# Kernel tuning notes

Hardware: AMD Instinct MI355X
Metric: run time of the kernel (lower is better)

Reference implementation:

```python
import jax, jax.numpy as jnp
import numpy as np

H, D, KD, E = 8, 128, 16, 128
B, G = 16, 501

def setup_inputs() -> dict:
    key = jax.random.key(0)
    ks = jax.random.split(key, 12)
    stdv = 1.0 / np.sqrt(KD)
    u = lambda k, shape, s: jax.random.uniform(k, shape, jnp.float32, -s, s)
    inp = {"q": jax.random.normal(ks[0], (B, G, D), jnp.float32)}
    names = ["W_query", "W_key", "W_val", "W1_query", "W2_query", "W3_query",
             "W4_query", "W5_query", "W6_query"]
    for i, n in enumerate(names):
        inp[n] = u(ks[i + 1], (H, D, KD), stdv)
    inp["W_out"] = u(ks[10], (H, KD, E), 1.0 / np.sqrt(E))
    return inp

def _forward(q, W_query, W_key, W_val, W1, W2, W3, W4, W5, W6, W_out):
    h = q  # self-attention: h defaults to q
    b, g, d = h.shape
    np_ = (g - 1) // 2
    norm = 1.0 / jnp.sqrt(jnp.float32(KD))
    pick = h[:, 1:np_ + 1]          # [b, np, d]
    delivery = h[:, np_ + 1:]       # [b, np, d]
    proj = lambda x, W: jnp.einsum('bnd,hdk->hbnk', x, W)
    Q = proj(q, W_query); K = proj(h, W_key); V = proj(h, W_val)
    K_pick = proj(pick, W_key); V_pick = proj(pick, W_val)
    K_del = proj(delivery, W_key); V_del = proj(delivery, W_val)
    Q_pick = proj(pick, W1); Q_pick_ap = proj(pick, W2); Q_pick_ad = proj(pick, W3)
    Q_del = proj(delivery, W4); Q_del_ad = proj(delivery, W5); Q_del_ap = proj(delivery, W6)

    comp = norm * jnp.einsum('hbqk,hbgk->hbqg', Q, K)                 # [h,b,g,g]
    c_pd = norm * jnp.sum(Q_pick * K_del, -1)                          # [h,b,np]
    c_p_ap = norm * jnp.einsum('hbqk,hbpk->hbqp', Q_pick_ap, K_pick)   # [h,b,np,np]
    c_p_ad = norm * jnp.einsum('hbqk,hbpk->hbqp', Q_pick_ad, K_del)
    c_dp = norm * jnp.sum(Q_del * K_pick, -1)                          # [h,b,np]
    c_d_ad = norm * jnp.einsum('hbqk,hbpk->hbqp', Q_del_ad, K_del)
    c_d_ap = norm * jnp.einsum('hbqk,hbpk->hbqp', Q_del_ap, K_pick)

    ninf = lambda *s: jnp.full(s, -jnp.inf, comp.dtype)
    # pad branch scores to query length g (depot row + wrong-subset rows = -inf)
    c_add_del = jnp.concatenate([ninf(H, b, 1), c_pd, ninf(H, b, np_)], -1)[..., None]            # [h,b,g,1]
    c_add_ap = jnp.concatenate([ninf(H, b, 1, np_), c_p_ap, ninf(H, b, np_, np_)], 2)             # [h,b,g,np]
    c_add_ad = jnp.concatenate([ninf(H, b, 1, np_), c_p_ad, ninf(H, b, np_, np_)], 2)
    c_add_pick = jnp.concatenate([ninf(H, b, 1), ninf(H, b, np_), c_dp], -1)[..., None]
    c_add_ad2 = jnp.concatenate([ninf(H, b, 1, np_), ninf(H, b, np_, np_), c_d_ad], 2)
    c_add_ap2 = jnp.concatenate([ninf(H, b, 1, np_), ninf(H, b, np_, np_), c_d_ap], 2)
    comp_full = jnp.concatenate([comp, c_add_del, c_add_ap, c_add_ad,
                                 c_add_pick, c_add_ad2, c_add_ap2], -1)  # [h,b,g,g+2+4*np]

    attn = jax.nn.softmax(comp_full, axis=-1)

    z = lambda *s: jnp.zeros(s, V.dtype)
    V_add_del = jnp.concatenate([z(H, b, 1, KD), V_del, z(H, b, np_, KD)], 2)   # [h,b,g,kd]
    V_add_pick = jnp.concatenate([z(H, b, 1, KD), z(H, b, np_, KD), V_pick], 2)

    mm = lambda a, v: jnp.einsum('hbqp,hbpk->hbqk', a, v)
    heads = mm(attn[..., :g], V)
    heads = heads + attn[..., g:g + 1] * V_add_del
    heads = heads + mm(attn[..., g + 1:g + 1 + np_], V_pick)
    heads = heads + mm(attn[..., g + 1 + np_:g + 1 + 2 * np_], V_del)
    heads = heads + attn[..., g + 1 + 2 * np_:g + 2 + 2 * np_] * V_add_pick
    heads = heads + mm(attn[..., g + 2 + 2 * np_:g + 2 + 3 * np_], V_del)
    heads = heads + mm(attn[..., g + 2 + 3 * np_:], V_pick)

    return jnp.einsum('hbnk,hke->bne', heads, W_out)

def reference(q, W_query, W_key, W_val, W1_query, W2_query, W3_query,
              W4_query, W5_query, W6_query, W_out):
    return _forward(q, W_query, W_key, W_val, W1_query, W2_query, W3_query,
                    W4_query, W5_query, W6_query, W_out)
```

## Files before the change

kernel.cpp:

```cpp
#include <hip/hip_runtime.h>

#define H_ 8
#define D_ 128
#define KD_ 16
#define E_ 128
#define B_ 16
#define G_ 501
#define NP_ 250
#define BN_ (B_*G_)

typedef __bf16 bf16x8 __attribute__((ext_vector_type(8)));
typedef float f32x4 __attribute__((ext_vector_type(4)));
typedef unsigned short u16x8 __attribute__((ext_vector_type(8)));
typedef unsigned short u16x4 __attribute__((ext_vector_type(4)));
typedef bf16x8 __attribute__((may_alias)) bf16x8_a;
typedef u16x8 __attribute__((may_alias)) u16x8_a;
typedef u16x4 __attribute__((may_alias)) u16x4_a;

__device__ __forceinline__ unsigned short f2bf(float f) {
  unsigned int u = __builtin_bit_cast(unsigned int, f);
  unsigned int r = u + 0x7FFFu + ((u >> 16) & 1u);
  return (unsigned short)(r >> 16);
}
__device__ __forceinline__ float bf2f(unsigned short u) {
  unsigned int v = ((unsigned int)u) << 16;
  return __builtin_bit_cast(float, v);
}

__global__ __launch_bounds__(256) void k_prep(
    const float* __restrict__ w0, const float* __restrict__ w1, const float* __restrict__ w2,
    const float* __restrict__ w3, const float* __restrict__ w4, const float* __restrict__ w5,
    const float* __restrict__ w6, const float* __restrict__ w7, const float* __restrict__ w8,
    unsigned short* __restrict__ wct, unsigned short* __restrict__ Pvt) {
  int i = blockIdx.x * 256 + threadIdx.x;
  if (i < H_*9*KD_*D_) {
    int d = i & 127; int t = i >> 7; int k = t & 15; t >>= 4;
    int wi = t % 9; int h = t / 9;
    const float* src = w0;
    switch (wi) {
      case 1: src = w1; break; case 2: src = w2; break; case 3: src = w3; break;
      case 4: src = w4; break; case 5: src = w5; break; case 6: src = w6; break;
      case 7: src = w7; break; case 8: src = w8; break; default: break;
    }
    wct[i] = f2bf(src[h*(D_*KD_) + d*KD_ + k]);
  }
  if (i < 128*16*19) {
    int s = i / 304; int r2 = i - s*304; int k = r2 / 19; int key = 501 + (r2 - k*19);
    Pvt[(size_t)s*8320 + k*520 + key] = 0;
  }
}

__global__ __launch_bounds__(256) void k_proj(const float* __restrict__ q,
                                              const unsigned short* __restrict__ wct,
                                              unsigned short* __restrict__ P,
                                              unsigned short* __restrict__ Pvt) {
  const int tid = threadIdx.x;
  const int lane = tid & 63;
  const int wv = tid >> 6;
  const int ln = lane & 15;
  const int quad = lane >> 4;
  const int b = blockIdx.y >> 3;
  const int nt = blockIdx.y & 7;
  const int cbase = blockIdx.x * 64;

  __shared__ __align__(16) unsigned short sA[64*136];
  __shared__ __align__(16) unsigned short sB[64*136];

  for (int i = tid; i < 1024; i += 256) {
    int rr = i >> 4, half = i & 15;
    int r = min(nt*64 + rr, G_ - 1);
    const float* src = q + (size_t)(b*G_ + r)*D_ + half*8;
    float4 f0 = ((const float4*)src)[0];
    float4 f1 = ((const float4*)src)[1];
    u16x8 v;
    v[0]=f2bf(f0.x); v[1]=f2bf(f0.y); v[2]=f2bf(f0.z); v[3]=f2bf(f0.w);
    v[4]=f2bf(f1.x); v[5]=f2bf(f1.y); v[6]=f2bf(f1.z); v[7]=f2bf(f1.w);
    *(u16x8*)(sA + rr*136 + half*8) = v;
  }
  for (int i = tid; i < 1024; i += 256) {
    int cc = i >> 4, half = i & 15;
    u16x8 v = *(const u16x8*)(wct + (size_t)(cbase + cc)*D_ + half*8);
    *(u16x8*)(sB + cc*136 + half*8) = v;
  }
  __syncthreads();

  bf16x8 a[4];
  #pragma unroll
  for (int ks = 0; ks < 4; ++ks)
    a[ks] = *(const bf16x8_a*)(sA + (wv*16 + ln)*136 + ks*32 + quad*8);

  #pragma unroll
  for (int ct = 0; ct < 4; ++ct) {
    f32x4 acc = {0.f,0.f,0.f,0.f};
    #pragma unroll
    for (int ks = 0; ks < 4; ++ks) {
      bf16x8 bb = *(const bf16x8_a*)(sB + (ct*16 + ln)*136 + ks*32 + quad*8);
      acc = __builtin_amdgcn_mfma_f32_16x16x32_bf16(a[ks], bb, acc, 0,0,0);
    }
    const int c = cbase + ct*16 + ln;
    const int h = c / 144; const int rem = c - h*144; const int w = rem >> 4; const int k = rem & 15;
    if (w == 2) {
      unsigned short* dstv = Pvt + (size_t)(h*B_ + b)*8320 + k*520;
      #pragma unroll
      for (int g = 0; g < 4; ++g) {
        const int nn = nt*64 + wv*16 + quad*4 + g;
        if (nn < G_) dstv[nn] = f2bf(acc[g]);
      }
    } else {
      const float sc = (w == 1) ? 1.0f : 0.25f;
      const size_t pb = ((size_t)((h*9 + w)*B_ + b)*G_)*KD_ + k;
      #pragma unroll
      for (int g = 0; g < 4; ++g) {
        const int nn = nt*64 + wv*16 + quad*4 + g;
        if (nn < G_) P[pb + (size_t)nn*KD_] = f2bf(acc[g]*sc);
      }
    }
  }
}

__device__ __forceinline__ f32x4 mf(bf16x8 a, bf16x8 b, f32x4 c) {
  return __builtin_amdgcn_mfma_f32_16x16x32_bf16(a, b, c, 0,0,0);
}

__device__ __forceinline__ void score_chunk(
    int c, bool up, bool dn, int cbuf,
    const unsigned short* sK, bf16x8 qa, bf16x8 qp, bf16x8 qdl,
    unsigned short* eb, float rv, float& esum, int ln, int quad)
{
  const f32x4 z4 = {0.f,0.f,0.f,0.f};
  bf16x8 k0 = {}, k1 = {};
  if (quad < 2) {
    const unsigned short* kp = sK + (c*32 + ln)*24 + quad*8;
    k0 = *(const bf16x8_a*)(kp);
    k1 = *(const bf16x8_a*)(kp + 384);
  }
  f32x4 sa0 = mf(k0, qa, z4), sa1 = mf(k1, qa, z4);
  f32x4 sp0 = z4, sp1 = z4, sd0 = z4, sd1 = z4;
  if (up) { sp0 = mf(k0, qp, z4);  sp1 = mf(k1, qp, z4); }
  if (dn) { sd0 = mf(k0, qdl, z4); sd1 = mf(k1, qdl, z4); }

  float el = 0.f;
  unsigned short ev[8];
  #pragma unroll
  for (int t = 0; t < 2; ++t) {
    #pragma unroll
    for (int rg = 0; rg < 4; ++rg) {
      float comp = __expf(t ? sa1[rg] : sa0[rg]);
      if (c == 15 && t == 1) comp *= (quad*4 + rg <= 4) ? 1.f : 0.f;
      float ex = 0.f;
      if (up) {
        float m = 1.f;
        if (c == 0 && t == 0 && rg == 0) m = (quad != 0) ? 1.f : 0.f;
        if (c == 7 && t == 1) m = (quad*4 + rg <= 10) ? 1.f : 0.f;
        ex += m * __expf(t ? sp1[rg] : sp0[rg]);
      }
      if (dn) {
        float m = 1.f;
        if (c == 7)  m = (t == 1 && quad*4 + rg >= 11) ? 1.f : 0.f;
        if (c == 15 && t == 1) m = (quad*4 + rg <= 4) ? 1.f : 0.f;
        ex += m * __expf(t ? sd1[rg] : sd0[rg]);
      }
      float e = comp + rv * ex;
      el += e;
      ev[t*4 + rg] = f2bf(e);
    }
  }
  esum += el;
  u16x4 w0, w1;
  w0[0]=ev[0]; w0[1]=ev[1]; w0[2]=ev[2]; w0[3]=ev[3];
  w1[0]=ev[4]; w1[1]=ev[5]; w1[2]=ev[6]; w1[3]=ev[7];
  unsigned short* base = eb + cbuf*640 + ln*40 + quad*4;
  *(u16x4_a*)(base)      = w0;
  *(u16x4_a*)(base + 16) = w1;
}

__global__ __launch_bounds__(256, 2) void k_attn(const unsigned short* __restrict__ P,
                                                 const unsigned short* __restrict__ Pvt,
                                                 unsigned short* __restrict__ headsb) {
  const int rt2 = blockIdx.x, b = blockIdx.y, h = blockIdx.z;
  const int tid = threadIdx.x;
  const int lane = tid & 63;
  const int wv = tid >> 6;
  const int ln = lane & 15;
  const int quad = lane >> 4;

  __shared__ __align__(16) unsigned short sK [512*24];
  __shared__ __align__(16) unsigned short sVt[16*520];
  __shared__ __align__(16) unsigned short sQ [8*1040];
  __shared__ __align__(16) unsigned short eBuf[4*2*640];

  const size_t slab = (size_t)G_*KD_;
  const unsigned short* Pk = P + ((size_t)(h*9+1)*B_ + b)*slab;
  const u16x8 vz = {0,0,0,0,0,0,0,0};

  for (int i = tid; i < 1024; i += 256) {
    int key = i >> 1, half = i & 1;
    u16x8 v = vz;
    if (key < G_) v = *(const u16x8*)(Pk + key*KD_ + half*8);
    *(u16x8*)(sK + key*24 + half*8) = v;
  }
  const unsigned short* pv = Pvt + (size_t)(h*B_ + b)*8320;
  for (int i = tid; i < 1040; i += 256)
    *(u16x8*)(sVt + i*8) = *(const u16x8*)(pv + i*8);
  for (int i = tid; i < 1040; i += 256) {
    int t = i / 520; int j2 = i - t*520;
    int arr = j2 / 130; int j = j2 - arr*130;
    int rr = j >> 1, half = j & 1;
    int r = (rt2*2 + t)*64 + rr;
    u16x8 v = vz;
    if (rr < 64 && r < G_) {
      bool pick = (r <= NP_);
      int w = (arr==0) ? 0 : (arr==1) ? (pick?4:8) : (arr==2) ? (pick?5:7) : (pick?3:6);
      v = *(const u16x8*)(P + ((size_t)(h*9+w)*B_ + b)*slab + (size_t)r*KD_ + half*8);
    }
    *(u16x8*)(sQ + (t*4+arr)*1040 + j*8) = v;
  }
  __syncthreads();

  unsigned short* eb = eBuf + wv*1280;

  for (int t = 0; t < 2; ++t) {
    const int r0 = (rt2*2 + t)*64;
    const unsigned short* sQt = sQ + t*4160;
    const int aoff = (wv*16 + ln)*16 + quad*8;
    bf16x8 qa  = *(const bf16x8_a*)(sQt + aoff);
    bf16x8 qp  = *(const bf16x8_a*)(sQt + 1040 + aoff);
    bf16x8 qdl = *(const bf16x8_a*)(sQt + 2080 + aoff);

    const int ra = r0 + wv*16 + ln;
    const float rv = (ra >= 1) ? 1.f : 0.f;

    f32x4 acc = {0.f,0.f,0.f,0.f};
    float esum = 0.f;

    #pragma unroll
    for (int p = 0; p < 8; ++p) {
      const int c0 = 2*p, c1 = c0 + 1;
      score_chunk(c0, c0 <= 7, c0 >= 7, 0, sK, qa, qp, qdl, eb, rv, esum, ln, quad);
      score_chunk(c1, c1 <= 7, c1 >= 7, 1, sK, qa, qp, qdl, eb, rv, esum, ln, quad);
      #pragma unroll
      for (int u = 0; u < 2; ++u) {
        bf16x8 Ef = *(const bf16x8_a*)(eb + u*640 + ln*40 + quad*8);
        bf16x8 Vf = *(const bf16x8_a*)(sVt + ln*520 + (c0+u)*32 + quad*8);
        acc = mf(Vf, Ef, acc);
      }
    }

    esum += __shfl_xor(esum, 16);
    esum += __shfl_xor(esum, 32);

    const unsigned short* qsp = sQt + 3120 + (wv*16 + ln)*16;
    const int kpair = (ra >= 1 && ra < G_) ? ((ra <= NP_) ? ra + NP_ : ra - NP_) : 0;
    const unsigned short* ksp = sK + kpair*24;
    u16x8 qs0 = *(const u16x8_a*)(qsp), qs1 = *(const u16x8_a*)(qsp + 8);
    u16x8 ks0 = *(const u16x8_a*)(ksp), ks1 = *(const u16x8_a*)(ksp + 8);
    float s = 0.f;
    #pragma unroll
    for (int kd = 0; kd < 8; ++kd) {
      s = fmaf(bf2f(qs0[kd]), bf2f(ks0[kd]), s);
      s = fmaf(bf2f(qs1[kd]), bf2f(ks1[kd]), s);
    }
    const float rvs = (ra >= 1 && ra < G_) ? 1.f : 0.f;
    const float esng = rvs * __expf(s);
    const float rcp = __builtin_amdgcn_rcpf(esum + esng);

    u16x4 ov;
    ov[0] = f2bf((acc[0] + esng * bf2f(sVt[(quad*4+0)*520 + kpair])) * rcp);
    ov[1] = f2bf((acc[1] + esng * bf2f(sVt[(quad*4+1)*520 + kpair])) * rcp);
    ov[2] = f2bf((acc[2] + esng * bf2f(sVt[(quad*4+2)*520 + kpair])) * rcp);
    ov[3] = f2bf((acc[3] + esng * bf2f(sVt[(quad*4+3)*520 + kpair])) * rcp);
    if (ra < G_)
      *(u16x4*)(headsb + ((size_t)(b*G_ + ra))*E_ + h*16 + quad*4) = ov;
  }
}

__global__ __launch_bounds__(256) void k_out(const unsigned short* __restrict__ headsb,
                                             const float* __restrict__ wout,
                                             float* __restrict__ out) {
  const int tid = threadIdx.x;
  const int lane = tid & 63;
  const int wv = tid >> 6;
  const int ln = lane & 15;
  const int quad = lane >> 4;
  const int base = blockIdx.x * 64;

  __shared__ __align__(16) unsigned short sWt[128*136];
  for (int i = tid; i < 16384; i += 256) {
    int k = i >> 7, e = i & 127;
    sWt[e*136 + k] = f2bf(wout[i]);
  }
  __syncthreads();

  const int row = min(base + wv*16 + ln, BN_ - 1);
  bf16x8 a[4];
  #pragma unroll
  for (int ks = 0; ks < 4; ++ks)
    a[ks] = *(const bf16x8_a*)(headsb + (size_t)row*E_ + ks*32 + quad*8);

  #pragma unroll
  for (int ct = 0; ct < 8; ++ct) {
    f32x4 acc = {0.f,0.f,0.f,0.f};
    #pragma unroll
    for (int ks = 0; ks < 4; ++ks) {
      bf16x8 bb = *(const bf16x8_a*)(sWt + (ct*16 + ln)*136 + ks*32 + quad*8);
      acc = __builtin_amdgcn_mfma_f32_16x16x32_bf16(a[ks], bb, acc, 0,0,0);
    }
    #pragma unroll
    for (int g = 0; g < 4; ++g) {
      const int r = base + wv*16 + quad*4 + g;
      if (r < BN_) out[(size_t)r*E_ + ct*16 + ln] = acc[g];
    }
  }
}

extern "C" void kernel_launch(void* const* d_in, const int* in_sizes, int n_in,
                              void* d_out, int out_size, void* d_ws, size_t ws_size,
                              hipStream_t stream) {
  const float* q = (const float*)d_in[0];
  const float* w0 = (const float*)d_in[1];
  const float* w1 = (const float*)d_in[2];
  const float* w2 = (const float*)d_in[3];
  const float* w3 = (const float*)d_in[4];
  const float* w4 = (const float*)d_in[5];
  const float* w5 = (const float*)d_in[6];
  const float* w6 = (const float*)d_in[7];
  const float* w7 = (const float*)d_in[8];
  const float* w8 = (const float*)d_in[9];
  const float* wout = (const float*)d_in[10];
  float* out = (float*)d_out;

  char* ws = (char*)d_ws;
  unsigned short* wct    = (unsigned short*)(ws);
  unsigned short* P      = (unsigned short*)(ws + 294912);
  unsigned short* Pvt    = (unsigned short*)(ws + 18763776);
  unsigned short* headsb = (unsigned short*)(ws + 20893696);

  k_prep<<<dim3(576), dim3(256), 0, stream>>>(w0,w1,w2,w3,w4,w5,w6,w7,w8, wct, Pvt);
  k_proj<<<dim3(18, 128), dim3(256), 0, stream>>>(q, wct, P, Pvt);
  k_attn<<<dim3(4, 16, 8), dim3(256), 0, stream>>>(P, Pvt, headsb);
  k_out<<<dim3(126), dim3(256), 0, stream>>>(headsb, wout, out);
}
```

Measured before the change: 123.4 us.

## Fuse all stages into one cooperative persistent kernel with grid syncs

Replaces the four separate launches (prep, projection, attention, output) with a single cooperative kernel of 256 blocks that walks the stages in order and separates them with grid-wide syncs. The q-to-bf16 conversion moves into the prep phase and is written to a new workspace buffer. The attention stage now stages score chunks through a single per-wave buffer instead of a double buffer. The aim is to remove launch overheads and inter-kernel gaps. The cost is that the grid is capped at 256 blocks, so the attention and projection tiles are looped over fewer blocks, and the grid syncs add latency.

```diff
diff --git a/kernel.cpp b/kernel.cpp
--- a/kernel.cpp
+++ b/kernel.cpp
@@ -1,4 +1,7 @@
 #include <hip/hip_runtime.h>
+#include <hip/hip_cooperative_groups.h>
+
+namespace cg = cooperative_groups;
 
 #define H_ 8
 #define D_ 128
@@ -27,103 +30,12 @@
   return __builtin_bit_cast(float, v);
 }
 
-__global__ __launch_bounds__(256) void k_prep(
-    const float* __restrict__ w0, const float* __restrict__ w1, const float* __restrict__ w2,
-    const float* __restrict__ w3, const float* __restrict__ w4, const float* __restrict__ w5,
-    const float* __restrict__ w6, const float* __restrict__ w7, const float* __restrict__ w8,
-    unsigned short* __restrict__ wct, unsigned short* __restrict__ Pvt) {
-  int i = blockIdx.x * 256 + threadIdx.x;
-  if (i < H_*9*KD_*D_) {
-    int d = i & 127; int t = i >> 7; int k = t & 15; t >>= 4;
-    int wi = t % 9; int h = t / 9;
-    const float* src = w0;
-    switch (wi) {
-      case 1: src = w1; break; case 2: src = w2; break; case 3: src = w3; break;
-      case 4: src = w4; break; case 5: src = w5; break; case 6: src = w6; break;
-      case 7: src = w7; break; case 8: src = w8; break; default: break;
-    }
-    wct[i] = f2bf(src[h*(D_*KD_) + d*KD_ + k]);
-  }
-  if (i < 128*16*19) {
-    int s = i / 304; int r2 = i - s*304; int k = r2 / 19; int key = 501 + (r2 - k*19);
-    Pvt[(size_t)s*8320 + k*520 + key] = 0;
-  }
-}
-
-__global__ __launch_bounds__(256) void k_proj(const float* __restrict__ q,
-                                              const unsigned short* __restrict__ wct,
-                                              unsigned short* __restrict__ P,
-                                              unsigned short* __restrict__ Pvt) {
-  const int tid = threadIdx.x;
-  const int lane = tid & 63;
-  const int wv = tid >> 6;
-  const int ln = lane & 15;
-  const int quad = lane >> 4;
-  const int b = blockIdx.y >> 3;
-  const int nt = blockIdx.y & 7;
-  const int cbase = blockIdx.x * 64;
-
-  __shared__ __align__(16) unsigned short sA[64*136];
-  __shared__ __align__(16) unsigned short sB[64*136];
-
-  for (int i = tid; i < 1024; i += 256) {
-    int rr = i >> 4, half = i & 15;
-    int r = min(nt*64 + rr, G_ - 1);
-    const float* src = q + (size_t)(b*G_ + r)*D_ + half*8;
-    float4 f0 = ((const float4*)src)[0];
-    float4 f1 = ((const float4*)src)[1];
-    u16x8 v;
-    v[0]=f2bf(f0.x); v[1]=f2bf(f0.y); v[2]=f2bf(f0.z); v[3]=f2bf(f0.w);
-    v[4]=f2bf(f1.x); v[5]=f2bf(f1.y); v[6]=f2bf(f1.z); v[7]=f2bf(f1.w);
-    *(u16x8*)(sA + rr*136 + half*8) = v;
-  }
-  for (int i = tid; i < 1024; i += 256) {
-    int cc = i >> 4, half = i & 15;
-    u16x8 v = *(const u16x8*)(wct + (size_t)(cbase + cc)*D_ + half*8);
-    *(u16x8*)(sB + cc*136 + half*8) = v;
-  }
-  __syncthreads();
-
-  bf16x8 a[4];
-  #pragma unroll
-  for (int ks = 0; ks < 4; ++ks)
-    a[ks] = *(const bf16x8_a*)(sA + (wv*16 + ln)*136 + ks*32 + quad*8);
-
-  #pragma unroll
-  for (int ct = 0; ct < 4; ++ct) {
-    f32x4 acc = {0.f,0.f,0.f,0.f};
-    #pragma unroll
-    for (int ks = 0; ks < 4; ++ks) {
-      bf16x8 bb = *(const bf16x8_a*)(sB + (ct*16 + ln)*136 + ks*32 + quad*8);
-      acc = __builtin_amdgcn_mfma_f32_16x16x32_bf16(a[ks], bb, acc, 0,0,0);
-    }
-    const int c = cbase + ct*16 + ln;
-    const int h = c / 144; const int rem = c - h*144; const int w = rem >> 4; const int k = rem & 15;
-    if (w == 2) {
-      unsigned short* dstv = Pvt + (size_t)(h*B_ + b)*8320 + k*520;
-      #pragma unroll
-      for (int g = 0; g < 4; ++g) {
-        const int nn = nt*64 + wv*16 + quad*4 + g;
-        if (nn < G_) dstv[nn] = f2bf(acc[g]);
-      }
-    } else {
-      const float sc = (w == 1) ? 1.0f : 0.25f;
-      const size_t pb = ((size_t)((h*9 + w)*B_ + b)*G_)*KD_ + k;
-      #pragma unroll
-      for (int g = 0; g < 4; ++g) {
-        const int nn = nt*64 + wv*16 + quad*4 + g;
-        if (nn < G_) P[pb + (size_t)nn*KD_] = f2bf(acc[g]*sc);
-      }
-    }
-  }
-}
-
 __device__ __forceinline__ f32x4 mf(bf16x8 a, bf16x8 b, f32x4 c) {
   return __builtin_amdgcn_mfma_f32_16x16x32_bf16(a, b, c, 0,0,0);
 }
 
 __device__ __forceinline__ void score_chunk(
-    int c, bool up, bool dn, int cbuf,
+    int c, bool up, bool dn,
     const unsigned short* sK, bf16x8 qa, bf16x8 qp, bf16x8 qdl,
     unsigned short* eb, float rv, float& esum, int ln, int quad)
 {
@@ -169,146 +81,253 @@
   u16x4 w0, w1;
   w0[0]=ev[0]; w0[1]=ev[1]; w0[2]=ev[2]; w0[3]=ev[3];
   w1[0]=ev[4]; w1[1]=ev[5]; w1[2]=ev[6]; w1[3]=ev[7];
-  unsigned short* base = eb + cbuf*640 + ln*40 + quad*4;
+  unsigned short* base = eb + ln*40 + quad*4;
   *(u16x4_a*)(base)      = w0;
   *(u16x4_a*)(base + 16) = w1;
 }
 
-__global__ __launch_bounds__(256, 2) void k_attn(const unsigned short* __restrict__ P,
-                                                 const unsigned short* __restrict__ Pvt,
-                                                 unsigned short* __restrict__ headsb) {
-  const int rt2 = blockIdx.x, b = blockIdx.y, h = blockIdx.z;
+__global__ __launch_bounds__(256, 2) void mega(
+    const float* __restrict__ q,
+    const float* __restrict__ w0, const float* __restrict__ w1, const float* __restrict__ w2,
+    const float* __restrict__ w3, const float* __restrict__ w4, const float* __restrict__ w5,
+    const float* __restrict__ w6, const float* __restrict__ w7, const float* __restrict__ w8,
+    const float* __restrict__ wout,
+    unsigned short* __restrict__ wct, unsigned short* __restrict__ qb,
+    unsigned short* __restrict__ P,   unsigned short* __restrict__ Pvt,
+    unsigned short* __restrict__ headsb, float* __restrict__ out)
+{
+  cg::grid_group gg = cg::this_grid();
+  const int blk = blockIdx.x;
   const int tid = threadIdx.x;
   const int lane = tid & 63;
   const int wv = tid >> 6;
   const int ln = lane & 15;
   const int quad = lane >> 4;
-
-  __shared__ __align__(16) unsigned short sK [512*24];
-  __shared__ __align__(16) unsigned short sVt[16*520];
-  __shared__ __align__(16) unsigned short sQ [8*1040];
-  __shared__ __align__(16) unsigned short eBuf[4*2*640];
-
-  const size_t slab = (size_t)G_*KD_;
-  const unsigned short* Pk = P + ((size_t)(h*9+1)*B_ + b)*slab;
-  const u16x8 vz = {0,0,0,0,0,0,0,0};
-
-  for (int i = tid; i < 1024; i += 256) {
-    int key = i >> 1, half = i & 1;
-    u16x8 v = vz;
-    if (key < G_) v = *(const u16x8*)(Pk + key*KD_ + half*8);
-    *(u16x8*)(sK + key*24 + half*8) = v;
-  }
-  const unsigned short* pv = Pvt + (size_t)(h*B_ + b)*8320;
-  for (int i = tid; i < 1040; i += 256)
-    *(u16x8*)(sVt + i*8) = *(const u16x8*)(pv + i*8);
-  for (int i = tid; i < 1040; i += 256) {
-    int t = i / 520; int j2 = i - t*520;
-    int arr = j2 / 130; int j = j2 - arr*130;
-    int rr = j >> 1, half = j & 1;
-    int r = (rt2*2 + t)*64 + rr;
-    u16x8 v = vz;
-    if (rr < 64 && r < G_) {
-      bool pick = (r <= NP_);
-      int w = (arr==0) ? 0 : (arr==1) ? (pick?4:8) : (arr==2) ? (pick?5:7) : (pick?3:6);
-      v = *(const u16x8*)(P + ((size_t)(h*9+w)*B_ + b)*slab + (size_t)r*KD_ + half*8);
-    }
-    *(u16x8*)(sQ + (t*4+arr)*1040 + j*8) = v;
-  }
-  __syncthreads();
-
-  unsigned short* eb = eBuf + wv*1280;
-
-  for (int t = 0; t < 2; ++t) {
-    const int r0 = (rt2*2 + t)*64;
-    const unsigned short* sQt = sQ + t*4160;
-    const int aoff = (wv*16 + ln)*16 + quad*8;
-    bf16x8 qa  = *(const bf16x8_a*)(sQt + aoff);
-    bf16x8 qp  = *(const bf16x8_a*)(sQt + 1040 + aoff);
-    bf16x8 qdl = *(const bf16x8_a*)(sQt + 2080 + aoff);
-
-    const int ra = r0 + wv*16 + ln;
-    const float rv = (ra >= 1) ? 1.f : 0.f;
-
-    f32x4 acc = {0.f,0.f,0.f,0.f};
-    float esum = 0.f;
-
+  const int gtid = blk*256 + tid;
+  const int T = 256*256;
+
+  __shared__ __align__(16) char smraw[62976];
+  unsigned short* const sm16 = (unsigned short*)smraw;
+
+  for (int i = gtid; i < H_*9*KD_*D_; i += T) {
+    int d = i & 127; int t = i >> 7; int k = t & 15; t >>= 4;
+    int wi = t % 9; int h = t / 9;
+    const float* src = w0;
+    switch (wi) {
+      case 1: src = w1; break; case 2: src = w2; break; case 3: src = w3; break;
+      case 4: src = w4; break; case 5: src = w5; break; case 6: src = w6; break;
+      case 7: src = w7; break; case 8: src = w8; break; default: break;
+    }
+    wct[i] = f2bf(src[h*(D_*KD_) + d*KD_ + k]);
+  }
+  for (int j = gtid; j < BN_*D_/8; j += T) {
+    const float* src = q + (size_t)j*8;
+    float4 f0 = ((const float4*)src)[0];
+    float4 f1 = ((const float4*)src)[1];
+    u16x8 v;
+    v[0]=f2bf(f0.x); v[1]=f2bf(f0.y); v[2]=f2bf(f0.z); v[3]=f2bf(f0.w);
+    v[4]=f2bf(f1.x); v[5]=f2bf(f1.y); v[6]=f2bf(f1.z); v[7]=f2bf(f1.w);
+    *(u16x8*)(qb + (size_t)j*8) = v;
+  }
+  for (int i = gtid; i < 128*16*19; i += T) {
+    int s = i / 304; int r2 = i - s*304; int k = r2 / 19; int key = 501 + (r2 - k*19);
+    Pvt[(size_t)s*8320 + k*520 + key] = 0;
+  }
+  gg.sync();
+
+  {
+    unsigned short* const sA = sm16;
+    unsigned short* const sB = sm16 + 64*136;
+    for (int ti = blk; ti < 2304; ti += 256) {
+      const int x = ti / 128;
+      const int y = ti - x*128;
+      const int b = y >> 3, nt = y & 7;
+      const int cbase = x*64;
+      __syncthreads();
+      for (int i = tid; i < 1024; i += 256) {
+        int rr = i >> 4, half = i & 15;
+        int r = min(nt*64 + rr, G_ - 1);
+        u16x8 v = *(const u16x8*)(qb + (size_t)(b*G_ + r)*D_ + half*8);
+        *(u16x8*)(sA + rr*136 + half*8) = v;
+      }
+      for (int i = tid; i < 1024; i += 256) {
+        int cc = i >> 4, half = i & 15;
+        u16x8 v = *(const u16x8*)(wct + (size_t)(cbase + cc)*D_ + half*8);
+        *(u16x8*)(sB + cc*136 + half*8) = v;
+      }
+      __syncthreads();
+
+      bf16x8 a[4];
+      #pragma unroll
+      for (int ks = 0; ks < 4; ++ks)
+        a[ks] = *(const bf16x8_a*)(sA + (wv*16 + ln)*136 + ks*32 + quad*8);
+
+      #pragma unroll
+      for (int ct = 0; ct < 4; ++ct) {
+        f32x4 acc = {0.f,0.f,0.f,0.f};
+        #pragma unroll
+        for (int ks = 0; ks < 4; ++ks) {
+          bf16x8 bb = *(const bf16x8_a*)(sB + (ct*16 + ln)*136 + ks*32 + quad*8);
+          acc = mf(a[ks], bb, acc);
+        }
+        const int c = cbase + ct*16 + ln;
+        const int h = c / 144; const int rem = c - h*144;
+        const int w = rem >> 4; const int k = rem & 15;
+        if (w == 2) {
+          unsigned short* dstv = Pvt + (size_t)(h*B_ + b)*8320 + k*520;
+          #pragma unroll
+          for (int g = 0; g < 4; ++g) {
+            const int nn = nt*64 + wv*16 + quad*4 + g;
+            if (nn < G_) dstv[nn] = f2bf(acc[g]);
+          }
+        } else {
+          const float sc = (w == 1) ? 1.0f : 0.25f;
+          const size_t pb = ((size_t)((h*9 + w)*B_ + b)*G_)*KD_ + k;
+          #pragma unroll
+          for (int g = 0; g < 4; ++g) {
+            const int nn = nt*64 + wv*16 + quad*4 + g;
+            if (nn < G_) P[pb + (size_t)nn*KD_] = f2bf(acc[g]*sc);
+          }
+        }
+      }
+    }
+  }
+  gg.sync();
+
+  {
+    unsigned short* const sK   = sm16;
+    unsigned short* const sVt  = sm16 + 12288;
+    unsigned short* const sQ   = sm16 + 20608;
+    unsigned short* const eBuf = sm16 + 28928;
+    const size_t slab = (size_t)G_*KD_;
+    const u16x8 vz = {0,0,0,0,0,0,0,0};
+
+    for (int u = blk; u < 512; u += 256) {
+      const int h = u >> 6;
+      const int b = (u >> 2) & 15;
+      const int rt2 = u & 3;
+      const unsigned short* Pk = P + ((size_t)(h*9+1)*B_ + b)*slab;
+
+      __syncthreads();
+      for (int i = tid; i < 1024; i += 256) {
+        int key = i >> 1, half = i & 1;
+        u16x8 v = vz;
+        if (key < G_) v = *(const u16x8*)(Pk + key*KD_ + half*8);
+        *(u16x8*)(sK + key*24 + half*8) = v;
+      }
+      const unsigned short* pv = Pvt + (size_t)(h*B_ + b)*8320;
+      for (int i = tid; i < 1040; i += 256)
+        *(u16x8*)(sVt + i*8) = *(const u16x8*)(pv + i*8);
+      for (int i = tid; i < 1040; i += 256) {
+        int t = i / 520; int j2 = i - t*520;
+        int arr = j2 / 130; int j = j2 - arr*130;
+        int rr = j >> 1, half = j & 1;
+        int r = (rt2*2 + t)*64 + rr;
+        u16x8 v = vz;
+        if (rr < 64 && r < G_) {
+          bool pick = (r <= NP_);
+          int w = (arr==0) ? 0 : (arr==1) ? (pick?4:8) : (arr==2) ? (pick?5:7) : (pick?3:6);
+          v = *(const u16x8*)(P + ((size_t)(h*9+w)*B_ + b)*slab + (size_t)r*KD_ + half*8);
+        }
+        *(u16x8*)(sQ + (t*4+arr)*1040 + j*8) = v;
+      }
+      __syncthreads();
+
+      unsigned short* eb = eBuf + wv*640;
+
+      for (int t = 0; t < 2; ++t) {
+        const int r0 = (rt2*2 + t)*64;
+        const unsigned short* sQt = sQ + t*4160;
+        const int aoff = (wv*16 + ln)*16 + quad*8;
+        bf16x8 qa  = *(const bf16x8_a*)(sQt + aoff);
+        bf16x8 qp  = *(const bf16x8_a*)(sQt + 1040 + aoff);
+        bf16x8 qdl = *(const bf16x8_a*)(sQt + 2080 + aoff);
+
+        const int ra = r0 + wv*16 + ln;
+        const float rv = (ra >= 1) ? 1.f : 0.f;
+
+        f32x4 acc = {0.f,0.f,0.f,0.f};
+        float esum = 0.f;
+
+        #pragma unroll
+        for (int c = 0; c < 7; ++c) {
+          score_chunk(c, true, false, sK, qa, qp, qdl, eb, rv, esum, ln, quad);
+          bf16x8 Ef = *(const bf16x8_a*)(eb + ln*40 + quad*8);
+          bf16x8 Vf = *(const bf16x8_a*)(sVt + ln*520 + c*32 + quad*8);
+          acc = mf(Vf, Ef, acc);
+        }
+        {
+          score_chunk(7, true, true, sK, qa, qp, qdl, eb, rv, esum, ln, quad);
+          bf16x8 Ef = *(const bf16x8_a*)(eb + ln*40 + quad*8);
+          bf16x8 Vf = *(const bf16x8_a*)(sVt + ln*520 + 7*32 + quad*8);
+          acc = mf(Vf, Ef, acc);
+        }
+        #pragma unroll
+        for (int c = 8; c < 16; ++c) {
+          score_chunk(c, false, true, sK, qa, qp, qdl, eb, rv, esum, ln, quad);
+          bf16x8 Ef = *(const bf16x8_a*)(eb + ln*40 + quad*8);
+          bf16x8 Vf = *(const bf16x8_a*)(sVt + ln*520 + c*32 + quad*8);
+          acc = mf(Vf, Ef, acc);
+        }
+
+        esum += __shfl_xor(esum, 16);
+        esum += __shfl_xor(esum, 32);
+
+        const unsigned short* qsp = sQt + 3120 + (wv*16 + ln)*16;
+        const int kpair = (ra >= 1 && ra < G_) ? ((ra <= NP_) ? ra + NP_ : ra - NP_) : 0;
+        const unsigned short* ksp = sK + kpair*24;
+        u16x8 qs0 = *(const u16x8_a*)(qsp), qs1 = *(const u16x8_a*)(qsp + 8);
+        u16x8 ks0 = *(const u16x8_a*)(ksp), ks1 = *(const u16x8_a*)(ksp + 8);
+        float s = 0.f;
+        #pragma unroll
+        for (int kd = 0; kd < 8; ++kd) {
+          s = fmaf(bf2f(qs0[kd]), bf2f(ks0[kd]), s);
+          s = fmaf(bf2f(qs1[kd]), bf2f(ks1[kd]), s);
+        }
+        const float rvs = (ra >= 1 && ra < G_) ? 1.f : 0.f;
+        const float esng = rvs * __expf(s);
+        const float rcp = __builtin_amdgcn_rcpf(esum + esng);
+
+        u16x4 ov;
+        ov[0] = f2bf((acc[0] + esng * bf2f(sVt[(quad*4+0)*520 + kpair])) * rcp);
+        ov[1] = f2bf((acc[1] + esng * bf2f(sVt[(quad*4+1)*520 + kpair])) * rcp);
+        ov[2] = f2bf((acc[2] + esng * bf2f(sVt[(quad*4+2)*520 + kpair])) * rcp);
+        ov[3] = f2bf((acc[3] + esng * bf2f(sVt[(quad*4+3)*520 + kpair])) * rcp);
+        if (ra < G_)
+          *(u16x4*)(headsb + ((size_t)(b*G_ + ra))*E_ + h*16 + quad*4) = ov;
+      }
+    }
+  }
+  gg.sync();
+
+  if (blk < 126) {
+    unsigned short* const sWt = sm16;
+    const int base = blk * 64;
+    for (int i = tid; i < 16384; i += 256) {
+      int k = i >> 7, e = i & 127;
+      sWt[e*136 + k] = f2bf(wout[i]);
+    }
+    __syncthreads();
+
+    const int row = min(base + wv*16 + ln, BN_ - 1);
+    bf16x8 a[4];
     #pragma unroll
-    for (int p = 0; p < 8; ++p) {
-      const int c0 = 2*p, c1 = c0 + 1;
-      score_chunk(c0, c0 <= 7, c0 >= 7, 0, sK, qa, qp, qdl, eb, rv, esum, ln, quad);
-      score_chunk(c1, c1 <= 7, c1 >= 7, 1, sK, qa, qp, qdl, eb, rv, esum, ln, quad);
+    for (int ks = 0; ks < 4; ++ks)
+      a[ks] = *(const bf16x8_a*)(headsb + (size_t)row*E_ + ks*32 + quad*8);
+
+    #pragma unroll
+    for (int ct = 0; ct < 8; ++ct) {
+      f32x4 acc = {0.f,0.f,0.f,0.f};
       #pragma unroll
-      for (int u = 0; u < 2; ++u) {
-        bf16x8 Ef = *(const bf16x8_a*)(eb + u*640 + ln*40 + quad*8);
-        bf16x8 Vf = *(const bf16x8_a*)(sVt + ln*520 + (c0+u)*32 + quad*8);
-        acc = mf(Vf, Ef, acc);
-      }
-    }
-
-    esum += __shfl_xor(esum, 16);
-    esum += __shfl_xor(esum, 32);
-
-    const unsigned short* qsp = sQt + 3120 + (wv*16 + ln)*16;
-    const int kpair = (ra >= 1 && ra < G_) ? ((ra <= NP_) ? ra + NP_ : ra - NP_) : 0;
-    const unsigned short* ksp = sK + kpair*24;
-    u16x8 qs0 = *(const u16x8_a*)(qsp), qs1 = *(const u16x8_a*)(qsp + 8);
-    u16x8 ks0 = *(const u16x8_a*)(ksp), ks1 = *(const u16x8_a*)(ksp + 8);
-    float s = 0.f;
-    #pragma unroll
-    for (int kd = 0; kd < 8; ++kd) {
-      s = fmaf(bf2f(qs0[kd]), bf2f(ks0[kd]), s);
-      s = fmaf(bf2f(qs1[kd]), bf2f(ks1[kd]), s);
-    }
-    const float rvs = (ra >= 1 && ra < G_) ? 1.f : 0.f;
-    const float esng = rvs * __expf(s);
-    const float rcp = __builtin_amdgcn_rcpf(esum + esng);
-
-    u16x4 ov;
-    ov[0] = f2bf((acc[0] + esng * bf2f(sVt[(quad*4+0)*520 + kpair])) * rcp);
-    ov[1] = f2bf((acc[1] + esng * bf2f(sVt[(quad*4+1)*520 + kpair])) * rcp);
-    ov[2] = f2bf((acc[2] + esng * bf2f(sVt[(quad*4+2)*520 + kpair])) * rcp);
-    ov[3] = f2bf((acc[3] + esng * bf2f(sVt[(quad*4+3)*520 + kpair])) * rcp);
-    if (ra < G_)
-      *(u16x4*)(headsb + ((size_t)(b*G_ + ra))*E_ + h*16 + quad*4) = ov;
-  }
-}
-
-__global__ __launch_bounds__(256) void k_out(const unsigned short* __restrict__ headsb,
-                                             const float* __restrict__ wout,
-                                             float* __restrict__ out) {
-  const int tid = threadIdx.x;
-  const int lane = tid & 63;
-  const int wv = tid >> 6;
-  const int ln = lane & 15;
-  const int quad = lane >> 4;
-  const int base = blockIdx.x * 64;
-
-  __shared__ __align__(16) unsigned short sWt[128*136];
-  for (int i = tid; i < 16384; i += 256) {
-    int k = i >> 7, e = i & 127;
-    sWt[e*136 + k] = f2bf(wout[i]);
-  }
-  __syncthreads();
-
-  const int row = min(base + wv*16 + ln, BN_ - 1);
-  bf16x8 a[4];
-  #pragma unroll
-  for (int ks = 0; ks < 4; ++ks)
-    a[ks] = *(const bf16x8_a*)(headsb + (size_t)row*E_ + ks*32 + quad*8);
-
-  #pragma unroll
-  for (int ct = 0; ct < 8; ++ct) {
-    f32x4 acc = {0.f,0.f,0.f,0.f};
-    #pragma unroll
-    for (int ks = 0; ks < 4; ++ks) {
-      bf16x8 bb = *(const bf16x8_a*)(sWt + (ct*16 + ln)*136 + ks*32 + quad*8);
-      acc = __builtin_amdgcn_mfma_f32_16x16x32_bf16(a[ks], bb, acc, 0,0,0);
-    }
-    #pragma unroll
-    for (int g = 0; g < 4; ++g) {
-      const int r = base + wv*16 + quad*4 + g;
-      if (r < BN_) out[(size_t)r*E_ + ct*16 + ln] = acc[g];
+      for (int ks = 0; ks < 4; ++ks) {
+        bf16x8 bb = *(const bf16x8_a*)(sWt + (ct*16 + ln)*136 + ks*32 + quad*8);
+        acc = mf(a[ks], bb, acc);
+      }
+      #pragma unroll
+      for (int g = 0; g < 4; ++g) {
+        const int r = base + wv*16 + quad*4 + g;
+        if (r < BN_) out[(size_t)r*E_ + ct*16 + ln] = acc[g];
+      }
     }
   }
 }
@@ -331,12 +350,15 @@
 
   char* ws = (char*)d_ws;
   unsigned short* wct    = (unsigned short*)(ws);
-  unsigned short* P      = (unsigned short*)(ws + 294912);
-  unsigned short* Pvt    = (unsigned short*)(ws + 18763776);
-  unsigned short* headsb = (unsigned short*)(ws + 20893696);
-
-  k_prep<<<dim3(576), dim3(256), 0, stream>>>(w0,w1,w2,w3,w4,w5,w6,w7,w8, wct, Pvt);
-  k_proj<<<dim3(18, 128), dim3(256), 0, stream>>>(q, wct, P, Pvt);
-  k_attn<<<dim3(4, 16, 8), dim3(256), 0, stream>>>(P, Pvt, headsb);
-  k_out<<<dim3(126), dim3(256), 0, stream>>>(headsb, wout, out);
-}
+  unsigned short* qb     = (unsigned short*)(ws + 294912);
+  unsigned short* P      = (unsigned short*)(ws + 2347008);
+  unsigned short* Pvt    = (unsigned short*)(ws + 20815872);
+  unsigned short* headsb = (unsigned short*)(ws + 22945792);
+
+  void* args[] = {
+    (void*)&q, (void*)&w0, (void*)&w1, (void*)&w2, (void*)&w3, (void*)&w4,
+    (void*)&w5, (void*)&w6, (void*)&w7, (void*)&w8, (void*)&wout,
+    (void*)&wct, (void*)&qb, (void*)&P, (void*)&Pvt, (void*)&headsb, (void*)&out
+  };
+  hipLaunchCooperativeKernel((const void*)mega, dim3(256), dim3(256), args, 0, stream);
+}
```

Result: slower. 255.9 us (+107.4%).
